# Performance work log

Hardware: AMD Instinct MI355X
Metric: run time of the kernel (lower is better)

Reference implementation:

```python
import jax, jax.numpy as jnp
import numpy as np

MARGIN = 10.0
ALPHA = 3.0
BETA = 0.3
GAMMA = 0.3


def setup_inputs() -> dict:
    key = jax.random.key(0)
    k1, k2 = jax.random.split(key)
    B, S, D = 256, 2048, 128
    return {
        "expert_concepts": jax.random.normal(k1, (B, S, D), dtype=jnp.float32),
        "violator_concepts": jax.random.normal(k2, (B, S, D), dtype=jnp.float32),
    }


def _pairwise_sqdist(a, b):
    # a: [Na, D], b: [Nb, D] -> [Na, Nb] squared euclidean distances
    sq = (jnp.sum(a * a, axis=1)[:, None]
          + jnp.sum(b * b, axis=1)[None, :]
          - 2.0 * a @ b.T)
    return jnp.maximum(sq, 0.0)


def reference(expert_concepts, violator_concepts):
    Be = expert_concepts.shape[0]
    Bv = violator_concepts.shape[0]

    expert_centroids = jnp.mean(expert_concepts, axis=1)      # [Be, D]
    violator_centroids = jnp.mean(violator_concepts, axis=1)  # [Bv, D]

    # Separation: mean over all (i, j) pairs of clamp(margin - ||e_i - v_j||)^2
    sq_ev = _pairwise_sqdist(expert_centroids, violator_centroids)
    dist_ev = jnp.sqrt(sq_ev + 1e-12)
    separation_loss = jnp.mean(jnp.maximum(MARGIN - dist_ev, 0.0) ** 2)

    # Clustering: mean over i<j of squared distances (sqrt then square == sq)
    def _cluster(c):
        n = c.shape[0]
        sq = _pairwise_sqdist(c, c)
        count = n * (n - 1) // 2
        # sum over i<j == total sum / 2 (matrix is symmetric, diag ~ 0)
        upper = jnp.triu(sq, k=1)
        return jnp.sum(upper) / count if count > 0 else jnp.float32(0.0)

    expert_clustering_loss = _cluster(expert_centroids)
    violator_clustering_loss = _cluster(violator_centroids)

    total_loss = (ALPHA * separation_loss
                  + BETA * expert_clustering_loss
                  + GAMMA * violator_clustering_loss)
    return total_loss
```

## Files before the change

kernel.cpp:

```cpp
#include <hip/hip_runtime.h>

typedef float f4 __attribute__((ext_vector_type(4)));

#define BB 256
#define SS 2048
#define DD 128
#define MARGIN 10.0f
#define ALPHA 3.0f
#define BETA 0.3f
#define GAMMA 0.3f

#define WS_CENT    0
#define WS_NORMS   65536
#define WS_PART    66048

__global__ __launch_bounds__(1024) void centroid_kernel(
    const float* __restrict__ E, const float* __restrict__ V,
    float* __restrict__ cent, float* __restrict__ norms)
{
    const int p = blockIdx.x;
    const float* src = (p < BB) ? (E + (size_t)p * SS * DD)
                                : (V + (size_t)(p - BB) * SS * DD);
    const f4* src4 = reinterpret_cast<const f4*>(src);

    const int tid  = threadIdx.x;
    const int d4   = tid & 31;
    const int ssub = tid >> 5;

    const f4* p4 = src4 + (size_t)ssub * 32 + d4;
    f4 a0 = 0.f, a1 = 0.f, a2 = 0.f, a3 = 0.f;
    #pragma unroll 2
    for (int it = 0; it < 16; ++it) {
        f4 x0 = __builtin_nontemporal_load(p4);
        f4 x1 = __builtin_nontemporal_load(p4 + 1024);
        f4 x2 = __builtin_nontemporal_load(p4 + 2048);
        f4 x3 = __builtin_nontemporal_load(p4 + 3072);
        a0 += x0; a1 += x1; a2 += x2; a3 += x3;
        p4 += 4096;
    }
    f4 acc = (a0 + a1) + (a2 + a3);

    acc.x += __shfl_down(acc.x, 32);
    acc.y += __shfl_down(acc.y, 32);
    acc.z += __shfl_down(acc.z, 32);
    acc.w += __shfl_down(acc.w, 32);

    __shared__ f4 red[512];
    const int wave = tid >> 6;
    const int lane = tid & 63;
    if (lane < 32) red[wave * 32 + lane] = acc;
    __syncthreads();
    for (int h = 8; h >= 1; h >>= 1) {
        if (tid < h * 32) red[tid] += red[tid + h * 32];
        __syncthreads();
    }

    __shared__ float nrm[32];
    if (tid < 32) {
        f4 c = red[tid] * (1.0f / (float)SS);
        reinterpret_cast<f4*>(cent)[p * 32 + tid] = c;
        nrm[tid] = c.x * c.x + c.y * c.y + c.z * c.z + c.w * c.w;
    }
    __syncthreads();
    if (tid == 0) {
        float n = 0.f;
        #pragma unroll
        for (int q = 0; q < 32; ++q) n += nrm[q];
        norms[p] = n;
    }
}

__global__ __launch_bounds__(256) void loss_kernel(
    const float* __restrict__ cent, const float* __restrict__ norms,
    float* __restrict__ partials)
{
    const int i = blockIdx.x;
    const int j = threadIdx.x;
    const f4* C4 = reinterpret_cast<const f4*>(cent);

    __shared__ f4 Ei[32];
    __shared__ f4 Vi[32];
    if (j < 32)       Ei[j]      = C4[i * 32 + j];
    else if (j < 64)  Vi[j - 32] = C4[(BB + i) * 32 + (j - 32)];
    __syncthreads();

    float dev = 0.f, dee = 0.f, dvv = 0.f;
    #pragma unroll 8
    for (int q = 0; q < 32; ++q) {
        const f4 e  = Ei[q];
        const f4 v  = Vi[q];
        const f4 ej = C4[j * 32 + q];
        const f4 vj = C4[(BB + j) * 32 + q];
        f4 t0 = e * vj; dev += t0.x + t0.y + t0.z + t0.w;
        f4 t1 = e * ej; dee += t1.x + t1.y + t1.z + t1.w;
        f4 t2 = v * vj; dvv += t2.x + t2.y + t2.z + t2.w;
    }

    const float ne_i = norms[i];
    const float nv_i = norms[BB + i];
    const float ne_j = norms[j];
    const float nv_j = norms[BB + j];

    float sq_ev = fmaxf(ne_i + nv_j - 2.0f * dev, 0.0f);
    float dist  = sqrtf(sq_ev + 1e-12f);
    float t     = fmaxf(MARGIN - dist, 0.0f);
    float sep   = t * t;

    float see = (j > i) ? fmaxf(ne_i + ne_j - 2.0f * dee, 0.0f) : 0.0f;
    float svv = (j > i) ? fmaxf(nv_i + nv_j - 2.0f * dvv, 0.0f) : 0.0f;

    #pragma unroll
    for (int off = 32; off >= 1; off >>= 1) {
        sep += __shfl_down(sep, off);
        see += __shfl_down(see, off);
        svv += __shfl_down(svv, off);
    }
    __shared__ float wred[4][3];
    if ((j & 63) == 0) {
        wred[j >> 6][0] = sep;
        wred[j >> 6][1] = see;
        wred[j >> 6][2] = svv;
    }
    __syncthreads();
    if (j == 0) {
        partials[i]          = wred[0][0] + wred[1][0] + wred[2][0] + wred[3][0];
        partials[BB + i]     = wred[0][1] + wred[1][1] + wred[2][1] + wred[3][1];
        partials[2 * BB + i] = wred[0][2] + wred[1][2] + wred[2][2] + wred[3][2];
    }
}

__global__ __launch_bounds__(256) void finalize_kernel(
    const float* __restrict__ partials, float* __restrict__ out)
{
    const int j = threadIdx.x;
    float s0 = partials[j];
    float s1 = partials[BB + j];
    float s2 = partials[2 * BB + j];
    #pragma unroll
    for (int off = 32; off >= 1; off >>= 1) {
        s0 += __shfl_down(s0, off);
        s1 += __shfl_down(s1, off);
        s2 += __shfl_down(s2, off);
    }
    __shared__ float wred[4][3];
    if ((j & 63) == 0) {
        wred[j >> 6][0] = s0;
        wred[j >> 6][1] = s1;
        wred[j >> 6][2] = s2;
    }
    __syncthreads();
    if (j == 0) {
        float sums0 = wred[0][0] + wred[1][0] + wred[2][0] + wred[3][0];
        float sums1 = wred[0][1] + wred[1][1] + wred[2][1] + wred[3][1];
        float sums2 = wred[0][2] + wred[1][2] + wred[2][2] + wred[3][2];
        const float sep_mean = sums0 / (float)(BB * BB);
        const float cnt      = (float)(BB * (BB - 1) / 2);
        out[0] = ALPHA * sep_mean + (BETA * sums1 + GAMMA * sums2) / cnt;
    }
}

extern "C" void kernel_launch(void* const* d_in, const int* in_sizes, int n_in,
                              void* d_out, int out_size, void* d_ws, size_t ws_size,
                              hipStream_t stream) {
    const float* E = (const float*)d_in[0];
    const float* V = (const float*)d_in[1];
    float* ws   = (float*)d_ws;
    float* cent = ws + WS_CENT;
    float* nrm  = ws + WS_NORMS;
    float* part = ws + WS_PART;
    float* out  = (float*)d_out;

    centroid_kernel<<<512, 1024, 0, stream>>>(E, V, cent, nrm);
    loss_kernel<<<BB, 256, 0, stream>>>(cent, nrm, part);
    finalize_kernel<<<1, 256, 0, stream>>>(part, out);
}
```

Measured before the change: 98.63 us.

## Compute clustering loss in closed form and fuse finalize via last-block atomic

Replaces the pairwise clustering distances with the identity sum_{i<j}||ci-cj||^2 = N*sum||ci||^2 - ||sum ci||^2, so the loss kernel only computes the expert-violator dot products. The separate finalize kernel is removed: each block writes its partial, bumps an atomic counter, and the last block performs the final reduction and clustering computation. This cuts per-thread work in the loss kernel and saves one kernel launch. The closed form can lose precision through cancellation, and the counter reset in the centroid kernel relies on stream ordering.

```diff
diff --git a/kernel.cpp b/kernel.cpp
--- a/kernel.cpp
+++ b/kernel.cpp
@@ -10,13 +10,15 @@
 #define BETA 0.3f
 #define GAMMA 0.3f
 
-#define WS_CENT    0
-#define WS_NORMS   65536
-#define WS_PART    66048
+#define WS_CENT   0
+#define WS_NORMS  65536
+#define WS_PART   66048
+#define WS_CNT    66304
 
 __global__ __launch_bounds__(1024) void centroid_kernel(
     const float* __restrict__ E, const float* __restrict__ V,
-    float* __restrict__ cent, float* __restrict__ norms)
+    float* __restrict__ cent, float* __restrict__ norms,
+    unsigned int* __restrict__ counter)
 {
     const int p = blockIdx.x;
     const float* src = (p < BB) ? (E + (size_t)p * SS * DD)
@@ -26,6 +28,8 @@
     const int tid  = threadIdx.x;
     const int d4   = tid & 31;
     const int ssub = tid >> 5;
+
+    if (p == 0 && tid == 0) *counter = 0u;
 
     const f4* p4 = src4 + (size_t)ssub * 32 + d4;
     f4 a0 = 0.f, a1 = 0.f, a2 = 0.f, a3 = 0.f;
@@ -46,116 +50,114 @@
     acc.w += __shfl_down(acc.w, 32);
 
     __shared__ f4 red[512];
-    const int wave = tid >> 6;
-    const int lane = tid & 63;
-    if (lane < 32) red[wave * 32 + lane] = acc;
+    if ((tid & 63) < 32) red[(tid >> 6) * 32 + (tid & 63)] = acc;
     __syncthreads();
     for (int h = 8; h >= 1; h >>= 1) {
         if (tid < h * 32) red[tid] += red[tid + h * 32];
         __syncthreads();
     }
 
-    __shared__ float nrm[32];
     if (tid < 32) {
         f4 c = red[tid] * (1.0f / (float)SS);
         reinterpret_cast<f4*>(cent)[p * 32 + tid] = c;
-        nrm[tid] = c.x * c.x + c.y * c.y + c.z * c.z + c.w * c.w;
-    }
-    __syncthreads();
-    if (tid == 0) {
-        float n = 0.f;
-        #pragma unroll
-        for (int q = 0; q < 32; ++q) n += nrm[q];
-        norms[p] = n;
+        float n = c.x * c.x + c.y * c.y + c.z * c.z + c.w * c.w;
+        n += __shfl_down(n, 16);
+        n += __shfl_down(n, 8);
+        n += __shfl_down(n, 4);
+        n += __shfl_down(n, 2);
+        n += __shfl_down(n, 1);
+        if (tid == 0) norms[p] = n;
     }
 }
 
-__global__ __launch_bounds__(256) void loss_kernel(
+__global__ __launch_bounds__(256) void sep_finalize_kernel(
     const float* __restrict__ cent, const float* __restrict__ norms,
-    float* __restrict__ partials)
+    float* __restrict__ partials, unsigned int* __restrict__ counter,
+    float* __restrict__ out)
 {
     const int i = blockIdx.x;
     const int j = threadIdx.x;
     const f4* C4 = reinterpret_cast<const f4*>(cent);
 
     __shared__ f4 Ei[32];
-    __shared__ f4 Vi[32];
-    if (j < 32)       Ei[j]      = C4[i * 32 + j];
-    else if (j < 64)  Vi[j - 32] = C4[(BB + i) * 32 + (j - 32)];
+    if (j < 32) Ei[j] = C4[i * 32 + j];
     __syncthreads();
 
-    float dev = 0.f, dee = 0.f, dvv = 0.f;
+    float dev = 0.f;
     #pragma unroll 8
     for (int q = 0; q < 32; ++q) {
         const f4 e  = Ei[q];
-        const f4 v  = Vi[q];
-        const f4 ej = C4[j * 32 + q];
         const f4 vj = C4[(BB + j) * 32 + q];
-        f4 t0 = e * vj; dev += t0.x + t0.y + t0.z + t0.w;
-        f4 t1 = e * ej; dee += t1.x + t1.y + t1.z + t1.w;
-        f4 t2 = v * vj; dvv += t2.x + t2.y + t2.z + t2.w;
+        f4 t0 = e * vj;
+        dev += t0.x + t0.y + t0.z + t0.w;
     }
+    float sq_ev = fmaxf(norms[i] + norms[BB + j] - 2.0f * dev, 0.0f);
+    float dist  = sqrtf(sq_ev + 1e-12f);
+    float tt    = fmaxf(MARGIN - dist, 0.0f);
+    float sep   = tt * tt;
 
-    const float ne_i = norms[i];
-    const float nv_i = norms[BB + i];
-    const float ne_j = norms[j];
-    const float nv_j = norms[BB + j];
+    #pragma unroll
+    for (int off = 32; off >= 1; off >>= 1) sep += __shfl_down(sep, off);
+    __shared__ float wred[4];
+    if ((j & 63) == 0) wred[j >> 6] = sep;
+    __syncthreads();
 
-    float sq_ev = fmaxf(ne_i + nv_j - 2.0f * dev, 0.0f);
-    float dist  = sqrtf(sq_ev + 1e-12f);
-    float t     = fmaxf(MARGIN - dist, 0.0f);
-    float sep   = t * t;
+    __shared__ unsigned int s_old;
+    if (j == 0) {
+        partials[i] = wred[0] + wred[1] + wred[2] + wred[3];
+        __threadfence();
+        s_old = atomicAdd(counter, 1u);
+    }
+    __syncthreads();
+    if (s_old != BB - 1) return;
 
-    float see = (j > i) ? fmaxf(ne_i + ne_j - 2.0f * dee, 0.0f) : 0.0f;
-    float svv = (j > i) ? fmaxf(nv_i + nv_j - 2.0f * dvv, 0.0f) : 0.0f;
+    __threadfence();
+
+    float a_e = norms[j];
+    float a_v = norms[BB + j];
+    float sp  = partials[j];
+
+    const float* base = (j < 128) ? cent : cent + BB * DD;
+    const int d = j & 127;
+    float cs = 0.f;
+    #pragma unroll 4
+    for (int ii = 0; ii < BB; ++ii) cs += base[ii * DD + d];
+    float cs2 = cs * cs;
+
+    __shared__ float sarr[256];
+    sarr[j] = cs2;
+    __syncthreads();
+    for (int h = 64; h >= 1; h >>= 1) {
+        if ((j & 127) < h) sarr[j] += sarr[j + h];
+        __syncthreads();
+    }
 
     #pragma unroll
     for (int off = 32; off >= 1; off >>= 1) {
-        sep += __shfl_down(sep, off);
-        see += __shfl_down(see, off);
-        svv += __shfl_down(svv, off);
+        a_e += __shfl_down(a_e, off);
+        a_v += __shfl_down(a_v, off);
+        sp  += __shfl_down(sp , off);
     }
-    __shared__ float wred[4][3];
+    __shared__ float w3[4][3];
     if ((j & 63) == 0) {
-        wred[j >> 6][0] = sep;
-        wred[j >> 6][1] = see;
-        wred[j >> 6][2] = svv;
+        w3[j >> 6][0] = a_e;
+        w3[j >> 6][1] = a_v;
+        w3[j >> 6][2] = sp;
     }
     __syncthreads();
+
     if (j == 0) {
-        partials[i]          = wred[0][0] + wred[1][0] + wred[2][0] + wred[3][0];
-        partials[BB + i]     = wred[0][1] + wred[1][1] + wred[2][1] + wred[3][1];
-        partials[2 * BB + i] = wred[0][2] + wred[1][2] + wred[2][2] + wred[3][2];
-    }
-}
+        float A_e = w3[0][0] + w3[1][0] + w3[2][0] + w3[3][0];
+        float A_v = w3[0][1] + w3[1][1] + w3[2][1] + w3[3][1];
+        float SP  = w3[0][2] + w3[1][2] + w3[2][2] + w3[3][2];
+        float B_e = sarr[0];
+        float B_v = sarr[128];
 
-__global__ __launch_bounds__(256) void finalize_kernel(
-    const float* __restrict__ partials, float* __restrict__ out)
-{
-    const int j = threadIdx.x;
-    float s0 = partials[j];
-    float s1 = partials[BB + j];
-    float s2 = partials[2 * BB + j];
-    #pragma unroll
-    for (int off = 32; off >= 1; off >>= 1) {
-        s0 += __shfl_down(s0, off);
-        s1 += __shfl_down(s1, off);
-        s2 += __shfl_down(s2, off);
-    }
-    __shared__ float wred[4][3];
-    if ((j & 63) == 0) {
-        wred[j >> 6][0] = s0;
-        wred[j >> 6][1] = s1;
-        wred[j >> 6][2] = s2;
-    }
-    __syncthreads();
-    if (j == 0) {
-        float sums0 = wred[0][0] + wred[1][0] + wred[2][0] + wred[3][0];
-        float sums1 = wred[0][1] + wred[1][1] + wred[2][1] + wred[3][1];
-        float sums2 = wred[0][2] + wred[1][2] + wred[2][2] + wred[3][2];
-        const float sep_mean = sums0 / (float)(BB * BB);
-        const float cnt      = (float)(BB * (BB - 1) / 2);
-        out[0] = ALPHA * sep_mean + (BETA * sums1 + GAMMA * sums2) / cnt;
+        const float cnt = (float)(BB * (BB - 1) / 2);
+        float ee_sum = fmaxf((float)BB * A_e - B_e, 0.0f);
+        float vv_sum = fmaxf((float)BB * A_v - B_v, 0.0f);
+        float sep_mean = SP / (float)(BB * BB);
+        out[0] = ALPHA * sep_mean + (BETA * ee_sum + GAMMA * vv_sum) / cnt;
     }
 }
 
@@ -168,9 +170,9 @@
     float* cent = ws + WS_CENT;
     float* nrm  = ws + WS_NORMS;
     float* part = ws + WS_PART;
+    unsigned int* cnt = (unsigned int*)(ws + WS_CNT);
     float* out  = (float*)d_out;
 
-    centroid_kernel<<<512, 1024, 0, stream>>>(E, V, cent, nrm);
-    loss_kernel<<<BB, 256, 0, stream>>>(cent, nrm, part);
-    finalize_kernel<<<1, 256, 0, stream>>>(part, out);
+    centroid_kernel<<<512, 1024, 0, stream>>>(E, V, cent, nrm, cnt);
+    sep_finalize_kernel<<<BB, 256, 0, stream>>>(cent, nrm, part, cnt, out);
 }
```

Result: slower. 114.4 us (+16.0%).
